# Kernel optimization log

Hardware: AMD Instinct MI355X
Metric: run time of the kernel (lower is better)

Reference implementation:

```python
import jax, jax.numpy as jnp
import numpy as np

HEADS = 4
HID = 128
NEG_SLOPE = 0.2  # PyG GATConv default leaky_relu slope
EPS = 1e-16      # PyG softmax denominator epsilon


def _gat_layer(x, src, dst, W, att_src, att_dst, bias, N):
    # x: [N, F_in]; W: [F_in, HEADS*HID]; att_*: [HEADS, HID]; bias: [HID]
    h = (x @ W).reshape(N, HEADS, HID)                 # [N, H, C]
    a_s = jnp.sum(h * att_src[None], axis=-1)          # [N, H]
    a_d = jnp.sum(h * att_dst[None], axis=-1)          # [N, H]
    alpha = jax.nn.leaky_relu(a_s[src] + a_d[dst], NEG_SLOPE)  # [E, H]
    # segment softmax over edges grouped by destination node
    amax = jax.ops.segment_max(alpha, dst, num_segments=N)     # [N, H]
    ex = jnp.exp(alpha - amax[dst])                             # [E, H]
    denom = jax.ops.segment_sum(ex, dst, num_segments=N)       # [N, H]
    alpha = ex / (denom[dst] + EPS)
    msg = h[src] * alpha[:, :, None]                            # [E, H, C]
    out = jax.ops.segment_sum(msg, dst, num_segments=N)        # [N, H, C]
    return out.mean(axis=1) + bias                              # concat=False -> mean over heads


def setup_inputs() -> dict:
    key = jax.random.key(0)
    ks = jax.random.split(key, 12)
    N, E, F_in = 50000, 400000, 256
    x = jax.random.normal(ks[0], (N, F_in), dtype=jnp.float32)
    edge_index = jax.random.randint(ks[1], (2, E), 0, N, dtype=jnp.int64)
    s1 = 1.0 / np.sqrt(F_in)
    s2 = 1.0 / np.sqrt(HID)
    return {
        "x": x,
        "edge_index": edge_index,
        "W1": jax.random.normal(ks[2], (F_in, HEADS * HID), dtype=jnp.float32) * s1,
        "att_src1": jax.random.normal(ks[3], (HEADS, HID), dtype=jnp.float32) * s2,
        "att_dst1": jax.random.normal(ks[4], (HEADS, HID), dtype=jnp.float32) * s2,
        "b1": jnp.zeros((HID,), dtype=jnp.float32),
        "W2": jax.random.normal(ks[5], (HID, HEADS * HID), dtype=jnp.float32) * s2,
        "att_src2": jax.random.normal(ks[6], (HEADS, HID), dtype=jnp.float32) * s2,
        "att_dst2": jax.random.normal(ks[7], (HEADS, HID), dtype=jnp.float32) * s2,
        "b2": jnp.zeros((HID,), dtype=jnp.float32),
    }


def reference(x, edge_index, W1, att_src1, att_dst1, b1, W2, att_src2, att_dst2, b2):
    N = x.shape[0]
    # PyG GATConv default add_self_loops=True
    loop = jnp.arange(N, dtype=edge_index.dtype)
    src = jnp.concatenate([edge_index[0], loop])
    dst = jnp.concatenate([edge_index[1], loop])
    h = jax.nn.relu(_gat_layer(x, src, dst, W1, att_src1, att_dst1, b1, N))
    h = jax.nn.relu(_gat_layer(h, src, dst, W2, att_src2, att_dst2, b2, N))
    # dropout is identity in eval mode
    return h
```

## Files before the change

### kernel.cpp

```cpp
#include <hip/hip_runtime.h>
#include <hip/hip_bf16.h>
#include <cstdint>

#define HEADS 4
#define HID 128
#define F_OUT 512
#define NEG_SLOPE 0.2f
#define GAT_EPS 1e-16f

typedef __attribute__((ext_vector_type(8))) short bf16x8;
typedef __attribute__((ext_vector_type(4))) float f32x4;

__device__ __forceinline__ float bf2f(unsigned short u) {
  unsigned int x = ((unsigned int)u) << 16;
  return __builtin_bit_cast(float, x);
}
__device__ __forceinline__ unsigned short f2b(float f) {
  unsigned int u = __builtin_bit_cast(unsigned int, f);
  unsigned int r = (u + 0x7fffu + ((u >> 16) & 1u)) >> 16;
  return (unsigned short)r;
}

__global__ __launch_bounds__(256) void detect_i64_kernel(const unsigned int* __restrict__ e,
                                                         int* __restrict__ flag) {
  __shared__ int nz;
  if (threadIdx.x == 0) nz = 0;
  __syncthreads();
  for (int i = threadIdx.x; i < 2048; i += blockDim.x) {
    if (e[2 * i + 1] != 0u) atomicOr(&nz, 1);
  }
  __syncthreads();
  if (threadIdx.x == 0) *flag = (nz == 0) ? 1 : 0;
}

__device__ __forceinline__ int edge_at(const int* __restrict__ e32,
                                       const long long* __restrict__ e64,
                                       int f, int i) {
  return f ? (int)e64[i] : e32[i];
}

__global__ __launch_bounds__(256) void hist_kernel(const int* __restrict__ e32,
                                                   const long long* __restrict__ e64,
                                                   const int* __restrict__ flag,
                                                   int* __restrict__ counts, int E, int N) {
  int i = blockIdx.x * 256 + threadIdx.x;
  int total = E + N;
  if (i >= total) return;
  int f = *flag;
  int dst = (i < E) ? edge_at(e32, e64, f, E + i) : (i - E);
  atomicAdd(&counts[dst], 1);
}

__global__ __launch_bounds__(256) void scan_partial_kernel(const int* __restrict__ counts,
                                                           int* __restrict__ partials, int N) {
  int t = threadIdx.x;
  int lane = t & 63, wv = t >> 6;
  int idx = blockIdx.x * 1024 + t * 4;
  int4 v = make_int4(0, 0, 0, 0);
  if (idx + 3 < N) v = *(const int4*)&counts[idx];
  else {
    if (idx + 0 < N) v.x = counts[idx + 0];
    if (idx + 1 < N) v.y = counts[idx + 1];
    if (idx + 2 < N) v.z = counts[idx + 2];
  }
  int s = v.x + v.y + v.z + v.w;
#pragma unroll
  for (int off = 32; off > 0; off >>= 1) s += __shfl_xor(s, off);
  __shared__ int wsum[4];
  if (lane == 0) wsum[wv] = s;
  __syncthreads();
  if (t == 0) partials[blockIdx.x] = wsum[0] + wsum[1] + wsum[2] + wsum[3];
}

__global__ __launch_bounds__(256) void scan_base_kernel(int* __restrict__ partials,
                                                        int* __restrict__ offsets,
                                                        int nblocks, int N) {
  __shared__ int buf[1024];
  int t = threadIdx.x;
  for (int i = t; i < nblocks; i += 256) buf[i] = partials[i];
  __syncthreads();
  if (t == 0) {
    int run = 0;
    for (int i = 0; i < nblocks; i++) { int c = buf[i]; buf[i] = run; run += c; }
    offsets[N] = run;
  }
  __syncthreads();
  for (int i = t; i < nblocks; i += 256) partials[i] = buf[i];
}

__global__ __launch_bounds__(256) void scan_final_kernel(const int* __restrict__ counts,
                                                         const int* __restrict__ partials,
                                                         int* __restrict__ offsets,
                                                         int* __restrict__ cursor, int N) {
  int t = threadIdx.x;
  int lane = t & 63, wv = t >> 6;
  int idx = blockIdx.x * 1024 + t * 4;
  int4 v = make_int4(0, 0, 0, 0);
  if (idx + 3 < N) v = *(const int4*)&counts[idx];
  else {
    if (idx + 0 < N) v.x = counts[idx + 0];
    if (idx + 1 < N) v.y = counts[idx + 1];
    if (idx + 2 < N) v.z = counts[idx + 2];
  }
  int s1 = v.x, s2 = s1 + v.y, s3 = s2 + v.z, s4 = s3 + v.w;
  int val = s4;
#pragma unroll
  for (int off = 1; off < 64; off <<= 1) {
    int y = __shfl_up(val, off);
    if (lane >= off) val += y;
  }
  __shared__ int wsum[4];
  if (lane == 63) wsum[wv] = val;
  __syncthreads();
  int wbase = 0;
  for (int i = 0; i < wv; i++) wbase += wsum[i];
  int excl = partials[blockIdx.x] + wbase + (val - s4);
  if (idx + 0 < N) { offsets[idx + 0] = excl;      cursor[idx + 0] = excl; }
  if (idx + 1 < N) { offsets[idx + 1] = excl + s1; cursor[idx + 1] = excl + s1; }
  if (idx + 2 < N) { offsets[idx + 2] = excl + s2; cursor[idx + 2] = excl + s2; }
  if (idx + 3 < N) { offsets[idx + 3] = excl + s3; cursor[idx + 3] = excl + s3; }
}

__global__ __launch_bounds__(256) void scatter_kernel(const int* __restrict__ e32,
                                                      const long long* __restrict__ e64,
                                                      const int* __restrict__ flag,
                                                      int* __restrict__ cursor,
                                                      int* __restrict__ csr_src,
                                                      int* __restrict__ csr_dst, int E, int N) {
  int i = blockIdx.x * 256 + threadIdx.x;
  int total = E + N;
  if (i >= total) return;
  int f = *flag;
  int src, dst;
  if (i < E) { src = edge_at(e32, e64, f, i); dst = edge_at(e32, e64, f, E + i); }
  else       { src = i - E; dst = src; }
  int pos = atomicAdd(&cursor[dst], 1);
  csr_src[pos] = src;
  csr_dst[pos] = dst;
}

__global__ __launch_bounds__(256) void cvt_x_kernel(const float* __restrict__ in,
                                                    unsigned short* __restrict__ out, long n4) {
  long i = (long)blockIdx.x * 256 + threadIdx.x;
  if (i >= n4) return;
  float4 v = *(const float4*)&in[i * 4];
  ushort4 o;
  o.x = f2b(v.x); o.y = f2b(v.y); o.z = f2b(v.z); o.w = f2b(v.w);
  *(ushort4*)&out[i * 4] = o;
}

__global__ __launch_bounds__(256) void cvt_w_kernel(const float* __restrict__ W,
                                                    unsigned short* __restrict__ Wt, int K) {
  int idx = blockIdx.x * 256 + threadIdx.x;
  if (idx >= K * F_OUT) return;
  int k = idx / F_OUT, c = idx % F_OUT;
  Wt[c * K + k] = f2b(W[idx]);
}

#define LDK 40
__global__ __launch_bounds__(256) void gemm_bf16_kernel(const unsigned short* __restrict__ A,
                                                        const unsigned short* __restrict__ Bt,
                                                        unsigned short* __restrict__ C,
                                                        int M, int K) {
  __shared__ unsigned short As[128][LDK];
  __shared__ unsigned short Bs[128][LDK];
  int tid = threadIdx.x;
  int lane = tid & 63, wid = tid >> 6;
  int wr = wid >> 1, wc = wid & 1;
  int rowBase = blockIdx.x * 128, colBase = blockIdx.y * 128;
  f32x4 acc[4][4];
#pragma unroll
  for (int i = 0; i < 4; i++)
#pragma unroll
    for (int j = 0; j < 4; j++) acc[i][j] = (f32x4){0.f, 0.f, 0.f, 0.f};

  int fr = lane & 15, fk = (lane >> 4) * 8;

  for (int k0 = 0; k0 < K; k0 += 32) {
#pragma unroll
    for (int i = 0; i < 2; i++) {
      int idx = i * 256 + tid;
      int r = idx >> 2, cq = (idx & 3) * 8;
      int gr = rowBase + r;
      float4 va = make_float4(0.f, 0.f, 0.f, 0.f);
      if (gr < M) va = *(const float4*)&A[(size_t)gr * K + k0 + cq];
      *(float4*)&As[r][cq] = va;
      *(float4*)&Bs[r][cq] = *(const float4*)&Bt[(size_t)(colBase + r) * K + k0 + cq];
    }
    __syncthreads();
    bf16x8 af[4], bfv[4];
#pragma unroll
    for (int mi = 0; mi < 4; mi++)
      af[mi] = *(const bf16x8*)&As[wr * 64 + mi * 16 + fr][fk];
#pragma unroll
    for (int ni = 0; ni < 4; ni++)
      bfv[ni] = *(const bf16x8*)&Bs[wc * 64 + ni * 16 + fr][fk];
#pragma unroll
    for (int mi = 0; mi < 4; mi++)
#pragma unroll
      for (int ni = 0; ni < 4; ni++)
        acc[mi][ni] = __builtin_amdgcn_mfma_f32_16x16x32_bf16(af[mi], bfv[ni], acc[mi][ni], 0, 0, 0);
    __syncthreads();
  }
  int r0 = rowBase + wr * 64, c0 = colBase + wc * 64;
#pragma unroll
  for (int mi = 0; mi < 4; mi++) {
#pragma unroll
    for (int ni = 0; ni < 4; ni++) {
      int col = c0 + ni * 16 + (lane & 15);
#pragma unroll
      for (int q = 0; q < 4; q++) {
        int row = r0 + mi * 16 + (lane >> 4) * 4 + q;
        if (row < M) C[(size_t)row * F_OUT + col] = f2b(acc[mi][ni][q]);
      }
    }
  }
}

__global__ __launch_bounds__(256) void attdot_kernel(const unsigned short* __restrict__ h,
                                                     const float* __restrict__ att_s,
                                                     const float* __restrict__ att_d,
                                                     float* __restrict__ a_s,
                                                     float* __restrict__ a_d, int N) {
  int lane = threadIdx.x & 63;
  int hh = lane >> 4, sl = lane & 15;
  int gwave = (blockIdx.x * 256 + threadIdx.x) >> 6;
  int nwaves = (gridDim.x * 256) >> 6;
  float asv[8], adv[8];
#pragma unroll
  for (int j = 0; j < 8; j++) {
    asv[j] = att_s[hh * HID + sl * 8 + j];
    adv[j] = att_d[hh * HID + sl * 8 + j];
  }
  for (int n = gwave; n < N; n += nwaves) {
    bf16x8 hv = *(const bf16x8*)&h[(size_t)n * F_OUT + hh * HID + sl * 8];
    float s = 0.f, d = 0.f;
#pragma unroll
    for (int j = 0; j < 8; j++) {
      float f = bf2f((unsigned short)hv[j]);
      s += f * asv[j];
      d += f * adv[j];
    }
#pragma unroll
    for (int off = 1; off < 16; off <<= 1) {
      s += __shfl_xor(s, off);
      d += __shfl_xor(d, off);
    }
    if (sl == 0) {
      a_s[n * HEADS + hh] = s;
      a_d[n * HEADS + hh] = d;
    }
  }
}

__global__ __launch_bounds__(256) void alpha_kernel(const int* __restrict__ csr_src,
                                                    const int* __restrict__ csr_dst,
                                                    const float* __restrict__ a_s,
                                                    const float* __restrict__ a_d,
                                                    float* __restrict__ alpha, int Etot) {
  int t = blockIdx.x * 256 + threadIdx.x;
  if (t >= Etot * HEADS) return;
  int i = t >> 2, hh = t & 3;
  int s = csr_src[i], d = csr_dst[i];
  float al = a_s[s * HEADS + hh] + a_d[d * HEADS + hh];
  al = (al > 0.f) ? al : al * NEG_SLOPE;
  alpha[t] = al;
}

__global__ __launch_bounds__(256) void norm_kernel(const int* __restrict__ offsets,
                                                   float* __restrict__ alpha, int N) {
  int t = blockIdx.x * 256 + threadIdx.x;
  if (t >= N * HEADS) return;
  int n = t >> 2, hh = t & 3;
  int beg = offsets[n], end = offsets[n + 1];
  float m = -1e30f;
  for (int i = beg; i < end; i++) m = fmaxf(m, alpha[i * HEADS + hh]);
  float denom = 0.f;
  for (int i = beg; i < end; i++) {
    float ex = __expf(alpha[i * HEADS + hh] - m);
    alpha[i * HEADS + hh] = ex;
    denom += ex;
  }
  float inv = 1.f / (denom + GAT_EPS);
  for (int i = beg; i < end; i++) alpha[i * HEADS + hh] *= inv;
}

template <int OUT_BF>
__global__ __launch_bounds__(256) void aggregate_kernel(const unsigned short* __restrict__ h,
                                                        const float* __restrict__ wexp,
                                                        const int* __restrict__ offsets,
                                                        const int* __restrict__ csr_src,
                                                        const float* __restrict__ bias,
                                                        void* __restrict__ out, int N) {
  int n = blockIdx.x;
  int w = threadIdx.x >> 6;
  int lane = threadIdx.x & 63;
  int slot = lane >> 4, sl = lane & 15;
  int beg = offsets[n], end = offsets[n + 1];

  float acc[8];
#pragma unroll
  for (int j = 0; j < 8; j++) acc[j] = 0.f;

  int e = beg + slot;
  int s = 0; float wgt = 0.f;
  if (e < end) { s = csr_src[e]; wgt = wexp[e * HEADS + w]; }
  while (e < end) {
    int ne = e + 4;
    int ns = 0; float nw = 0.f;
    if (ne < end) { ns = csr_src[ne]; nw = wexp[ne * HEADS + w]; }
    bf16x8 hv = *(const bf16x8*)&h[(size_t)s * F_OUT + w * HID + sl * 8];
#pragma unroll
    for (int j = 0; j < 8; j++) acc[j] += bf2f((unsigned short)hv[j]) * wgt;
    e = ne; s = ns; wgt = nw;
  }
#pragma unroll
  for (int j = 0; j < 8; j++) {
    acc[j] += __shfl_xor(acc[j], 16);
    acc[j] += __shfl_xor(acc[j], 32);
  }

  __shared__ float red[HEADS][HID];
  if (slot == 0) {
#pragma unroll
    for (int j = 0; j < 8; j++) red[w][sl * 8 + j] = acc[j];
  }
  __syncthreads();
  if (threadIdx.x < HID) {
    int c = threadIdx.x;
    float v = (red[0][c] + red[1][c] + red[2][c] + red[3][c]) * 0.25f + bias[c];
    v = fmaxf(v, 0.f);
    if (OUT_BF)
      ((unsigned short*)out)[(size_t)n * HID + c] = f2b(v);
    else
      ((float*)out)[(size_t)n * HID + c] = v;
  }
}

extern "C" void kernel_launch(void* const* d_in, const int* in_sizes, int n_in,
                              void* d_out, int out_size, void* d_ws, size_t ws_size,
                              hipStream_t stream) {
  const float* x   = (const float*)d_in[0];
  const int* e32   = (const int*)d_in[1];
  const long long* e64 = (const long long*)d_in[1];
  const float* W1  = (const float*)d_in[2];
  const float* as1 = (const float*)d_in[3];
  const float* ad1 = (const float*)d_in[4];
  const float* b1  = (const float*)d_in[5];
  const float* W2  = (const float*)d_in[6];
  const float* as2 = (const float*)d_in[7];
  const float* ad2 = (const float*)d_in[8];
  const float* b2  = (const float*)d_in[9];

  int F_in = in_sizes[2] / F_OUT;
  int N = in_sizes[0] / F_in;
  int E = in_sizes[1] / 2;
  int Etot = E + N;

  char* ws = (char*)d_ws;
  size_t off = 0;
  auto alloc = [&](size_t bytes) -> void* {
    void* p = ws + off;
    off = (off + bytes + 255) & ~(size_t)255;
    return p;
  };
  unsigned short* h_bf   = (unsigned short*)alloc((size_t)N * F_OUT * 2);
  unsigned short* x_bf   = (unsigned short*)alloc((size_t)N * F_in * 2);
  unsigned short* out1_bf= (unsigned short*)alloc((size_t)N * HID * 2);
  unsigned short* Wt1    = (unsigned short*)alloc((size_t)F_in * F_OUT * 2);
  unsigned short* Wt2    = (unsigned short*)alloc((size_t)HID * F_OUT * 2);
  float* a_s    = (float*)alloc((size_t)N * HEADS * 4);
  float* a_d    = (float*)alloc((size_t)N * HEADS * 4);
  float* alpha  = (float*)alloc((size_t)Etot * HEADS * 4);
  int* counts   = (int*)alloc((size_t)(N + 1) * 4);
  int* offsets  = (int*)alloc((size_t)(N + 1) * 4);
  int* cursor   = (int*)alloc((size_t)N * 4);
  int* csr_src  = (int*)alloc((size_t)Etot * 4);
  int* csr_dst  = (int*)alloc((size_t)Etot * 4);
  int* partials = (int*)alloc(1024 * 4);
  int* flag     = (int*)alloc(256);
  if (off > ws_size) return;

  int nchunks = (N + 1023) / 1024;

  hipMemsetAsync(counts, 0, (size_t)N * 4, stream);
  detect_i64_kernel<<<1, 256, 0, stream>>>((const unsigned int*)d_in[1], flag);
  hist_kernel<<<(Etot + 255) / 256, 256, 0, stream>>>(e32, e64, flag, counts, E, N);
  scan_partial_kernel<<<nchunks, 256, 0, stream>>>(counts, partials, N);
  scan_base_kernel<<<1, 256, 0, stream>>>(partials, offsets, nchunks, N);
  scan_final_kernel<<<nchunks, 256, 0, stream>>>(counts, partials, offsets, cursor, N);
  scatter_kernel<<<(Etot + 255) / 256, 256, 0, stream>>>(e32, e64, flag, cursor, csr_src, csr_dst, E, N);

  long n4x = (long)N * F_in / 4;
  cvt_x_kernel<<<(int)((n4x + 255) / 256), 256, 0, stream>>>(x, x_bf, n4x);
  cvt_w_kernel<<<(F_in * F_OUT + 255) / 256, 256, 0, stream>>>(W1, Wt1, F_in);
  cvt_w_kernel<<<(HID * F_OUT + 255) / 256, 256, 0, stream>>>(W2, Wt2, HID);

  dim3 ggrid((N + 127) / 128, F_OUT / 128);
  int ablocks = (Etot * HEADS + 255) / 256;
  int nblocks = (N * HEADS + 255) / 256;
  gemm_bf16_kernel<<<ggrid, 256, 0, stream>>>(x_bf, Wt1, h_bf, N, F_in);
  attdot_kernel<<<512, 256, 0, stream>>>(h_bf, as1, ad1, a_s, a_d, N);
  alpha_kernel<<<ablocks, 256, 0, stream>>>(csr_src, csr_dst, a_s, a_d, alpha, Etot);
  norm_kernel<<<nblocks, 256, 0, stream>>>(offsets, alpha, N);
  aggregate_kernel<1><<<N, 256, 0, stream>>>(h_bf, alpha, offsets, csr_src, b1, out1_bf, N);
  gemm_bf16_kernel<<<ggrid, 256, 0, stream>>>(out1_bf, Wt2, h_bf, N, HID);
  attdot_kernel<<<512, 256, 0, stream>>>(h_bf, as2, ad2, a_s, a_d, N);
  alpha_kernel<<<ablocks, 256, 0, stream>>>(csr_src, csr_dst, a_s, a_d, alpha, Etot);
  norm_kernel<<<nblocks, 256, 0, stream>>>(offsets, alpha, N);
  aggregate_kernel<0><<<N, 256, 0, stream>>>(h_bf, alpha, offsets, csr_src, b2, d_out, N);
}
```

Measured before the change: 379.0 us.

## Fuse attention dot into GEMM epilogue, fold x conversion and alpha into norm

The GEMM now computes per-head attention scores a_s/a_d in its epilogue by reducing the accumulator tiles against att vectors, which removes the separate attdot pass that re-read h. The layer-1 GEMM converts fp32 x to bf16 on load, dropping the cvt_x kernel and the bf16 copy of x. The alpha kernel and csr_dst array are removed; the norm kernel computes leaky-relu logits inline from csr_src and a_s. The trade-offs are extra shuffles and shared-memory reduction in the GEMM epilogue, doubled global read bytes for A in layer 1, and more gather work inside the serial per-node norm loop.

```diff
diff --git a/kernel.cpp b/kernel.cpp
--- a/kernel.cpp
+++ b/kernel.cpp
@@ -125,8 +125,7 @@
                                                       const long long* __restrict__ e64,
                                                       const int* __restrict__ flag,
                                                       int* __restrict__ cursor,
-                                                      int* __restrict__ csr_src,
-                                                      int* __restrict__ csr_dst, int E, int N) {
+                                                      int* __restrict__ csr_src, int E, int N) {
   int i = blockIdx.x * 256 + threadIdx.x;
   int total = E + N;
   if (i >= total) return;
@@ -136,17 +135,6 @@
   else       { src = i - E; dst = src; }
   int pos = atomicAdd(&cursor[dst], 1);
   csr_src[pos] = src;
-  csr_dst[pos] = dst;
-}
-
-__global__ __launch_bounds__(256) void cvt_x_kernel(const float* __restrict__ in,
-                                                    unsigned short* __restrict__ out, long n4) {
-  long i = (long)blockIdx.x * 256 + threadIdx.x;
-  if (i >= n4) return;
-  float4 v = *(const float4*)&in[i * 4];
-  ushort4 o;
-  o.x = f2b(v.x); o.y = f2b(v.y); o.z = f2b(v.z); o.w = f2b(v.w);
-  *(ushort4*)&out[i * 4] = o;
 }
 
 __global__ __launch_bounds__(256) void cvt_w_kernel(const float* __restrict__ W,
@@ -158,16 +146,24 @@
 }
 
 #define LDK 40
-__global__ __launch_bounds__(256) void gemm_bf16_kernel(const unsigned short* __restrict__ A,
-                                                        const unsigned short* __restrict__ Bt,
-                                                        unsigned short* __restrict__ C,
-                                                        int M, int K) {
+template <int AF32>
+__global__ __launch_bounds__(256) void gemm_att_kernel(const void* __restrict__ Araw,
+                                                       const unsigned short* __restrict__ Bt,
+                                                       unsigned short* __restrict__ C,
+                                                       const float* __restrict__ att_s,
+                                                       const float* __restrict__ att_d,
+                                                       float* __restrict__ a_s,
+                                                       float* __restrict__ a_d,
+                                                       int M, int K) {
   __shared__ unsigned short As[128][LDK];
   __shared__ unsigned short Bs[128][LDK];
+  __shared__ float sred[2][128];
+  __shared__ float dred[2][128];
   int tid = threadIdx.x;
   int lane = tid & 63, wid = tid >> 6;
   int wr = wid >> 1, wc = wid & 1;
-  int rowBase = blockIdx.x * 128, colBase = blockIdx.y * 128;
+  int head = blockIdx.y;
+  int rowBase = blockIdx.x * 128, colBase = head * 128;
   f32x4 acc[4][4];
 #pragma unroll
   for (int i = 0; i < 4; i++)
@@ -182,9 +178,25 @@
       int idx = i * 256 + tid;
       int r = idx >> 2, cq = (idx & 3) * 8;
       int gr = rowBase + r;
-      float4 va = make_float4(0.f, 0.f, 0.f, 0.f);
-      if (gr < M) va = *(const float4*)&A[(size_t)gr * K + k0 + cq];
-      *(float4*)&As[r][cq] = va;
+      if (AF32) {
+        const float* Af = (const float*)Araw;
+        float4 v0 = make_float4(0.f, 0.f, 0.f, 0.f), v1 = v0;
+        if (gr < M) {
+          v0 = *(const float4*)&Af[(size_t)gr * K + k0 + cq];
+          v1 = *(const float4*)&Af[(size_t)gr * K + k0 + cq + 4];
+        }
+        bf16x8 o;
+        o[0] = (short)f2b(v0.x); o[1] = (short)f2b(v0.y);
+        o[2] = (short)f2b(v0.z); o[3] = (short)f2b(v0.w);
+        o[4] = (short)f2b(v1.x); o[5] = (short)f2b(v1.y);
+        o[6] = (short)f2b(v1.z); o[7] = (short)f2b(v1.w);
+        *(bf16x8*)&As[r][cq] = o;
+      } else {
+        const unsigned short* Ab = (const unsigned short*)Araw;
+        float4 va = make_float4(0.f, 0.f, 0.f, 0.f);
+        if (gr < M) va = *(const float4*)&Ab[(size_t)gr * K + k0 + cq];
+        *(float4*)&As[r][cq] = va;
+      }
       *(float4*)&Bs[r][cq] = *(const float4*)&Bt[(size_t)(colBase + r) * K + k0 + cq];
     }
     __syncthreads();
@@ -202,6 +214,7 @@
         acc[mi][ni] = __builtin_amdgcn_mfma_f32_16x16x32_bf16(af[mi], bfv[ni], acc[mi][ni], 0, 0, 0);
     __syncthreads();
   }
+
   int r0 = rowBase + wr * 64, c0 = colBase + wc * 64;
 #pragma unroll
   for (int mi = 0; mi < 4; mi++) {
@@ -215,66 +228,63 @@
       }
     }
   }
-}
-
-__global__ __launch_bounds__(256) void attdot_kernel(const unsigned short* __restrict__ h,
-                                                     const float* __restrict__ att_s,
-                                                     const float* __restrict__ att_d,
-                                                     float* __restrict__ a_s,
-                                                     float* __restrict__ a_d, int N) {
-  int lane = threadIdx.x & 63;
-  int hh = lane >> 4, sl = lane & 15;
-  int gwave = (blockIdx.x * 256 + threadIdx.x) >> 6;
-  int nwaves = (gridDim.x * 256) >> 6;
-  float asv[8], adv[8];
-#pragma unroll
-  for (int j = 0; j < 8; j++) {
-    asv[j] = att_s[hh * HID + sl * 8 + j];
-    adv[j] = att_d[hh * HID + sl * 8 + j];
-  }
-  for (int n = gwave; n < N; n += nwaves) {
-    bf16x8 hv = *(const bf16x8*)&h[(size_t)n * F_OUT + hh * HID + sl * 8];
-    float s = 0.f, d = 0.f;
-#pragma unroll
-    for (int j = 0; j < 8; j++) {
-      float f = bf2f((unsigned short)hv[j]);
-      s += f * asv[j];
-      d += f * adv[j];
+
+  float asv[4], adv[4];
+#pragma unroll
+  for (int ni = 0; ni < 4; ni++) {
+    int cih = wc * 64 + ni * 16 + (lane & 15);
+    asv[ni] = att_s[head * HID + cih];
+    adv[ni] = att_d[head * HID + cih];
+  }
+#pragma unroll
+  for (int mi = 0; mi < 4; mi++) {
+#pragma unroll
+    for (int q = 0; q < 4; q++) {
+      float ps = 0.f, pd = 0.f;
+#pragma unroll
+      for (int ni = 0; ni < 4; ni++) {
+        ps += acc[mi][ni][q] * asv[ni];
+        pd += acc[mi][ni][q] * adv[ni];
+      }
+#pragma unroll
+      for (int off = 1; off < 16; off <<= 1) {
+        ps += __shfl_xor(ps, off);
+        pd += __shfl_xor(pd, off);
+      }
+      if ((lane & 15) == 0) {
+        int rl = wr * 64 + mi * 16 + (lane >> 4) * 4 + q;
+        sred[wc][rl] = ps;
+        dred[wc][rl] = pd;
+      }
     }
-#pragma unroll
-    for (int off = 1; off < 16; off <<= 1) {
-      s += __shfl_xor(s, off);
-      d += __shfl_xor(d, off);
+  }
+  __syncthreads();
+  if (tid < 128) {
+    int row = rowBase + tid;
+    if (row < M) {
+      a_s[row * HEADS + head] = sred[0][tid] + sred[1][tid];
+      a_d[row * HEADS + head] = dred[0][tid] + dred[1][tid];
     }
-    if (sl == 0) {
-      a_s[n * HEADS + hh] = s;
-      a_d[n * HEADS + hh] = d;
-    }
-  }
-}
-
-__global__ __launch_bounds__(256) void alpha_kernel(const int* __restrict__ csr_src,
-                                                    const int* __restrict__ csr_dst,
-                                                    const float* __restrict__ a_s,
-                                                    const float* __restrict__ a_d,
-                                                    float* __restrict__ alpha, int Etot) {
-  int t = blockIdx.x * 256 + threadIdx.x;
-  if (t >= Etot * HEADS) return;
-  int i = t >> 2, hh = t & 3;
-  int s = csr_src[i], d = csr_dst[i];
-  float al = a_s[s * HEADS + hh] + a_d[d * HEADS + hh];
-  al = (al > 0.f) ? al : al * NEG_SLOPE;
-  alpha[t] = al;
+  }
 }
 
 __global__ __launch_bounds__(256) void norm_kernel(const int* __restrict__ offsets,
+                                                   const int* __restrict__ csr_src,
+                                                   const float* __restrict__ a_s,
+                                                   const float* __restrict__ a_d,
                                                    float* __restrict__ alpha, int N) {
   int t = blockIdx.x * 256 + threadIdx.x;
   if (t >= N * HEADS) return;
   int n = t >> 2, hh = t & 3;
   int beg = offsets[n], end = offsets[n + 1];
+  float adn = a_d[n * HEADS + hh];
   float m = -1e30f;
-  for (int i = beg; i < end; i++) m = fmaxf(m, alpha[i * HEADS + hh]);
+  for (int i = beg; i < end; i++) {
+    float al = a_s[csr_src[i] * HEADS + hh] + adn;
+    al = (al > 0.f) ? al : al * NEG_SLOPE;
+    alpha[i * HEADS + hh] = al;
+    m = fmaxf(m, al);
+  }
   float denom = 0.f;
   for (int i = beg; i < end; i++) {
     float ex = __expf(alpha[i * HEADS + hh] - m);
@@ -365,7 +375,6 @@
     return p;
   };
   unsigned short* h_bf   = (unsigned short*)alloc((size_t)N * F_OUT * 2);
-  unsigned short* x_bf   = (unsigned short*)alloc((size_t)N * F_in * 2);
   unsigned short* out1_bf= (unsigned short*)alloc((size_t)N * HID * 2);
   unsigned short* Wt1    = (unsigned short*)alloc((size_t)F_in * F_OUT * 2);
   unsigned short* Wt2    = (unsigned short*)alloc((size_t)HID * F_OUT * 2);
@@ -376,7 +385,6 @@
   int* offsets  = (int*)alloc((size_t)(N + 1) * 4);
   int* cursor   = (int*)alloc((size_t)N * 4);
   int* csr_src  = (int*)alloc((size_t)Etot * 4);
-  int* csr_dst  = (int*)alloc((size_t)Etot * 4);
   int* partials = (int*)alloc(1024 * 4);
   int* flag     = (int*)alloc(256);
   if (off > ws_size) return;
@@ -389,24 +397,17 @@
   scan_partial_kernel<<<nchunks, 256, 0, stream>>>(counts, partials, N);
   scan_base_kernel<<<1, 256, 0, stream>>>(partials, offsets, nchunks, N);
   scan_final_kernel<<<nchunks, 256, 0, stream>>>(counts, partials, offsets, cursor, N);
-  scatter_kernel<<<(Etot + 255) / 256, 256, 0, stream>>>(e32, e64, flag, cursor, csr_src, csr_dst, E, N);
-
-  long n4x = (long)N * F_in / 4;
-  cvt_x_kernel<<<(int)((n4x + 255) / 256), 256, 0, stream>>>(x, x_bf, n4x);
+  scatter_kernel<<<(Etot + 255) / 256, 256, 0, stream>>>(e32, e64, flag, cursor, csr_src, E, N);
+
   cvt_w_kernel<<<(F_in * F_OUT + 255) / 256, 256, 0, stream>>>(W1, Wt1, F_in);
   cvt_w_kernel<<<(HID * F_OUT + 255) / 256, 256, 0, stream>>>(W2, Wt2, HID);
 
-  dim3 ggrid((N + 127) / 128, F_OUT / 128);
-  int ablocks = (Etot * HEADS + 255) / 256;
+  dim3 ggrid((N + 127) / 128, HEADS);
   int nblocks = (N * HEADS + 255) / 256;
-  gemm_bf16_kernel<<<ggrid, 256, 0, stream>>>(x_bf, Wt1, h_bf, N, F_in);
-  attdot_kernel<<<512, 256, 0, stream>>>(h_bf, as1, ad1, a_s, a_d, N);
-  alpha_kernel<<<ablocks, 256, 0, stream>>>(csr_src, csr_dst, a_s, a_d, alpha, Etot);
-  norm_kernel<<<nblocks, 256, 0, stream>>>(offsets, alpha, N);
+  gemm_att_kernel<1><<<ggrid, 256, 0, stream>>>(x, Wt1, h_bf, as1, ad1, a_s, a_d, N, F_in);
+  norm_kernel<<<nblocks, 256, 0, stream>>>(offsets, csr_src, a_s, a_d, alpha, N);
   aggregate_kernel<1><<<N, 256, 0, stream>>>(h_bf, alpha, offsets, csr_src, b1, out1_bf, N);
-  gemm_bf16_kernel<<<ggrid, 256, 0, stream>>>(out1_bf, Wt2, h_bf, N, HID);
-  attdot_kernel<<<512, 256, 0, stream>>>(h_bf, as2, ad2, a_s, a_d, N);
-  alpha_kernel<<<ablocks, 256, 0, stream>>>(csr_src, csr_dst, a_s, a_d, alpha, Etot);
-  norm_kernel<<<nblocks, 256, 0, stream>>>(offsets, alpha, N);
+  gemm_att_kernel<0><<<ggrid, 256, 0, stream>>>(out1_bf, Wt2, h_bf, as2, ad2, a_s, a_d, N, HID);
+  norm_kernel<<<nblocks, 256, 0, stream>>>(offsets, csr_src, a_s, a_d, alpha, N);
   aggregate_kernel<0><<<N, 256, 0, stream>>>(h_bf, alpha, offsets, csr_src, b2, d_out, N);
 }
```

After: 358.4 us. 1.06x faster.
